# Optimization experiments

Hardware: AMD Instinct MI355X
Metric: run time of the kernel (lower is better)

The kernel has to match this reference:

```python
import jax, jax.numpy as jnp
import numpy as np

B, P, ENC = 64, 196, 512
E, H, A, V, L = 1024, 1024, 512, 20000, 25


def setup_inputs() -> dict:
    key = jax.random.key(0)
    ks = jax.random.split(key, 20)
    s = 0.02
    return {
        "encoder_out": jax.random.normal(ks[0], (B, P, ENC), jnp.float32),
        "captions": jax.random.randint(ks[1], (B, L), 0, V),
        "lengths": L,
        # attention MLP
        "W_enc_att": jax.random.normal(ks[2], (ENC, A), jnp.float32) * s,
        "b_enc_att": jnp.zeros((A,), jnp.float32),
        "W_dec_att": jax.random.normal(ks[3], (H, A), jnp.float32) * s,
        "b_dec_att": jnp.zeros((A,), jnp.float32),
        "W_full_att": jax.random.normal(ks[4], (A, 1), jnp.float32) * s,
        "b_full_att": jnp.zeros((1,), jnp.float32),
        # embedding
        "emb_table": jax.random.normal(ks[5], (V, E), jnp.float32) * s,
        # LSTMCell: input = embedding + context -> (E+ENC, 4H)
        "W_ih": jax.random.normal(ks[6], (E + ENC, 4 * H), jnp.float32) * s,
        "b_ih": jnp.zeros((4 * H,), jnp.float32),
        "W_hh": jax.random.normal(ks[7], (H, 4 * H), jnp.float32) * s,
        "b_hh": jnp.zeros((4 * H,), jnp.float32),
        # init states
        "W_init_h": jax.random.normal(ks[8], (ENC, H), jnp.float32) * s,
        "b_init_h": jnp.zeros((H,), jnp.float32),
        "W_init_c": jax.random.normal(ks[9], (ENC, H), jnp.float32) * s,
        "b_init_c": jnp.zeros((H,), jnp.float32),
        # gate + output proj
        "W_fbeta": jax.random.normal(ks[10], (H, ENC), jnp.float32) * s,
        "b_fbeta": jnp.zeros((ENC,), jnp.float32),
        "W_fc": jax.random.normal(ks[11], (H, V), jnp.float32) * s,
        "b_fc": jnp.zeros((V,), jnp.float32),
    }


def _decode(encoder_out, W_enc_att, b_enc_att, W_dec_att, b_dec_att,
            W_full_att, b_full_att, emb_table, W_ih, b_ih, W_hh, b_hh,
            W_init_h, b_init_h, W_init_c, b_init_c, W_fbeta, b_fbeta,
            W_fc, b_fc, captions, T):
    # precompute encoder-side attention projection (constant across timesteps)
    att_enc = encoder_out @ W_enc_att + b_enc_att          # (B, P, A)
    mean_feat = encoder_out.mean(axis=1)                   # (B, ENC)
    h0 = mean_feat @ W_init_h + b_init_h
    c0 = mean_feat @ W_init_c + b_init_c
    embeddings = emb_table[captions[:, :T]]                # (B, T, E)
    xs = jnp.swapaxes(embeddings, 0, 1)                    # (T, B, E)

    def step(carry, emb_t):
        h, c = carry
        att_dec = h @ W_dec_att + b_dec_att                # (B, A)
        energy = (jax.nn.relu(att_enc + att_dec[:, None, :]) @ W_full_att
                  + b_full_att)[..., 0]                    # (B, P)
        alpha = jax.nn.softmax(energy, axis=1)
        context = jnp.einsum('bp,bpe->be', alpha, encoder_out)
        gate = jax.nn.sigmoid(h @ W_fbeta + b_fbeta)       # (B, ENC)
        x = jnp.concatenate([emb_t, gate * context], axis=1)
        gates = x @ W_ih + b_ih + h @ W_hh + b_hh          # (B, 4H)
        i, f, g, o = jnp.split(gates, 4, axis=1)           # torch order i,f,g,o
        c = jax.nn.sigmoid(f) * c + jax.nn.sigmoid(i) * jnp.tanh(g)
        h = jax.nn.sigmoid(o) * jnp.tanh(c)
        preds = h @ W_fc + b_fc                            # dropout = identity (eval)
        return (h, c), (preds, alpha)

    _, (preds, alphas) = jax.lax.scan(step, (h0, c0), xs)
    predictions = jnp.swapaxes(preds, 0, 1)                # (B, T, V)
    alphas = jnp.swapaxes(alphas, 0, 1)                    # (B, T, P)
    return predictions, alphas


def reference(encoder_out, captions, lengths, W_enc_att, b_enc_att, W_dec_att,
              b_dec_att, W_full_att, b_full_att, emb_table, W_ih, b_ih, W_hh,
              b_hh, W_init_h, b_init_h, W_init_c, b_init_c, W_fbeta, b_fbeta,
              W_fc, b_fc):
    T = int(lengths) - 1
    return _decode(encoder_out, W_enc_att, b_enc_att, W_dec_att, b_dec_att,
                   W_full_att, b_full_att, emb_table, W_ih, b_ih, W_hh, b_hh,
                   W_init_h, b_init_h, W_init_c, b_init_c, W_fbeta, b_fbeta,
                   W_fc, b_fc, captions, T)
```

## Files before the change

### kernel.cpp

```cpp
#include <hip/hip_runtime.h>
#include <hip/hip_bf16.h>

#define BB 64
#define PP 196
#define ENCD 512
#define ED 1024
#define HD 1024
#define AD 512
#define VD 20000
#define TT 24
#define VPAD 20096
#define HOFF 32768

typedef __attribute__((ext_vector_type(8))) short short8;
typedef __attribute__((ext_vector_type(4))) short short4v;
typedef __attribute__((ext_vector_type(4))) float f32x4;

__device__ __forceinline__ float sigf(float x) { return 1.f / (1.f + __expf(-x)); }

__device__ __forceinline__ unsigned short f2bf(float f) {
    unsigned u = __builtin_bit_cast(unsigned, f);
    u = (u + 0x7FFFu + ((u >> 16) & 1u)) >> 16;
    return (unsigned short)u;
}
__device__ __forceinline__ void split2(float v, unsigned short& h, unsigned short& l) {
    h = f2bf(v);
    float hf = __builtin_bit_cast(float, ((unsigned)h) << 16);
    l = f2bf(v - hf);
}

__global__ __launch_bounds__(256) void split_w_kernel(
    const float* __restrict__ W, unsigned short* __restrict__ oh,
    unsigned short* __restrict__ ol, int N , int Npad, int coff,
    int Nlaunch, int rowoff, int perm) {
    int n = blockIdx.x * 256 + threadIdx.x;
    if (n >= Nlaunch) return;
    int kc = blockIdx.y;
    int src = perm ? ((n & 3) * 1024 + (n >> 2)) : n;
    short8 vh, vl;
    #pragma unroll
    for (int j = 0; j < 8; ++j) {
        float v = (src < N) ? W[(size_t)(rowoff + kc * 8 + j) * N + src] : 0.f;
        unsigned short h, l; split2(v, h, l);
        vh[j] = (short)h; vl[j] = (short)l;
    }
    size_t o = ((size_t)kc * Npad + coff + n) * 8;
    *(short8*)(oh + o) = vh; *(short8*)(ol + o) = vl;
}

__global__ __launch_bounds__(256) void embed_f32_kernel(
    const int* __restrict__ captions, const float* __restrict__ table,
    float* __restrict__ emb_f) {
    int t = blockIdx.x, b = blockIdx.y;
    int tok = captions[b * 25 + t];
    const float4* src = (const float4*)(table + (size_t)tok * ED);
    float4* dst = (float4*)(emb_f + ((size_t)t * BB + b) * ED);
    dst[threadIdx.x] = src[threadIdx.x];
}

__global__ __launch_bounds__(256) void bias_perm_kernel(
    const float* __restrict__ b_ih, const float* __restrict__ b_hh,
    float* __restrict__ out) {
    int n = blockIdx.x * 256 + threadIdx.x;
    int src = (n & 3) * 1024 + (n >> 2);
    out[n] = b_ih[src] + b_hh[src];
}

__global__ __launch_bounds__(512) void mean_kernel(const float* __restrict__ enc,
                                                   float* __restrict__ mf) {
    int b = blockIdx.x; int e = threadIdx.x;
    const float* base = enc + (size_t)b * PP * ENCD + e;
    float s = 0.f;
    #pragma unroll 4
    for (int p = 0; p < PP; ++p) s += base[(size_t)p * ENCD];
    mf[b * ENCD + e] = s * (1.f / PP);
}

__global__ __launch_bounds__(256) void init_hc_kernel(
    const float* __restrict__ mf,
    const float* __restrict__ Wh, const float* __restrict__ bh,
    const float* __restrict__ Wc, const float* __restrict__ bc,
    unsigned short* __restrict__ hc_h, unsigned short* __restrict__ hc_l,
    float* __restrict__ c0) {
    int b = blockIdx.x;
    int isC = blockIdx.y;
    const float* W    = isC ? Wc : Wh;
    const float* bias = isC ? bc : bh;
    __shared__ float smf[ENCD];
    for (int i = threadIdx.x; i < ENCD; i += 256) smf[i] = mf[b * ENCD + i];
    __syncthreads();
    #pragma unroll
    for (int jj = 0; jj < 4; ++jj) {
        int j = threadIdx.x + jj * 256;
        float acc = bias[j];
        for (int k = 0; k < ENCD; ++k) acc += smf[k] * W[(size_t)k * HD + j];
        if (isC) c0[b * HD + j] = acc;
        else {
            unsigned short h, l; split2(acc, h, l);
            size_t o = ((size_t)(j >> 3) * 64 + b) * 8 + (j & 7);
            hc_h[o] = h; hc_l[o] = l;
        }
    }
}

__global__ __launch_bounds__(256) void mfma_gemm_bigf(
    const float* __restrict__ Ap,
    const unsigned short* __restrict__ Bh, const unsigned short* __restrict__ Bl,
    const float* __restrict__ bias, float* __restrict__ C,
    int N, int Npad, int K, int Mtiles, int Ntiles, int inner_m) {
    __shared__ __align__(16) short lds[32768];
    short* Ahs = lds;
    short* Als = lds + 8192;
    short* Bhs = lds + 16384;
    short* Bls = lds + 24576;
    int tid = threadIdx.x, lane = tid & 63, w = tid >> 6;
    int nwg = Mtiles * Ntiles;
    int orig = blockIdx.x;
    int q = nwg >> 3, r = nwg & 7;
    int xcd = orig & 7;
    int basew = (xcd < r) ? xcd * (q + 1) : r * (q + 1) + (xcd - r) * q;
    int wg = basew + (orig >> 3);
    int mt, nt;
    if (inner_m) { mt = wg % Mtiles; nt = wg / Mtiles; }
    else         { nt = wg % Ntiles; mt = wg / Ntiles; }
    int m0 = mt * 128, n0 = nt * 128;
    int wr = w >> 1, wc = w & 1;
    f32x4 acc[4][4];
    #pragma unroll
    for (int i = 0; i < 4; ++i)
        #pragma unroll
        for (int j = 0; j < 4; ++j) acc[i][j] = (f32x4){0.f, 0.f, 0.f, 0.f};
    int nsteps = K >> 6;
    float4 va[8];
    short8 rb[2][4];
    auto load_step = [&](int s) {
        int k0 = s * 64, kc0 = s * 8;
        #pragma unroll
        for (int it = 0; it < 8; ++it) {
            int idx = it * 256 + tid; int m = idx >> 4, k4 = idx & 15;
            va[it] = *(const float4*)(Ap + (size_t)(m0 + m) * K + k0 + k4 * 4);
        }
        #pragma unroll
        for (int it = 0; it < 4; ++it) {
            int g = w * 4 + it; int kcl = g >> 1; int rb0 = (g & 1) * 64;
            size_t gb = ((size_t)(kc0 + kcl) * Npad + n0 + rb0 + lane) * 8;
            rb[0][it] = *(const short8*)(Bh + gb);
            rb[1][it] = *(const short8*)(Bl + gb);
        }
    };
    load_step(0);
    for (int s = 0; s < nsteps; ++s) {
        __syncthreads();
        #pragma unroll
        for (int it = 0; it < 8; ++it) {
            int idx = it * 256 + tid; int m = idx >> 4, k4 = idx & 15;
            int kc = k4 >> 1, jh = (k4 & 1) * 4;
            float vv[4] = {va[it].x, va[it].y, va[it].z, va[it].w};
            short4v hv, lv;
            #pragma unroll
            for (int qq = 0; qq < 4; ++qq) {
                unsigned short h, l; split2(vv[qq], h, l);
                hv[qq] = (short)h; lv[qq] = (short)l;
            }
            int o = kc * 1024 + ((m ^ kc) << 3) + jh;
            *(short4v*)(Ahs + o) = hv;
            *(short4v*)(Als + o) = lv;
        }
        #pragma unroll
        for (int it = 0; it < 4; ++it) {
            int g = w * 4 + it; int kcl = g >> 1; int rb0 = (g & 1) * 64;
            int o = (kcl * 128 + rb0 + lane) * 8;
            *(short8*)(Bhs + o) = rb[0][it];
            *(short8*)(Bls + o) = rb[1][it];
        }
        __syncthreads();
        if (s + 1 < nsteps) load_step(s + 1);
        #pragma unroll
        for (int ks = 0; ks < 2; ++ks) {
            int kq = ks * 4 + (lane >> 4);
            short8 afh[4], afl[4], bfh[4], bfl[4];
            #pragma unroll
            for (int mi = 0; mi < 4; ++mi) {
                int row = wr * 64 + mi * 16 + (lane & 15);
                int o = kq * 1024 + ((row ^ kq) << 3);
                afh[mi] = *(const short8*)(Ahs + o);
                afl[mi] = *(const short8*)(Als + o);
            }
            #pragma unroll
            for (int ni = 0; ni < 4; ++ni) {
                int o = (kq * 128 + wc * 64 + ni * 16 + (lane & 15)) * 8;
                bfh[ni] = *(const short8*)(Bhs + o);
                bfl[ni] = *(const short8*)(Bls + o);
            }
            #pragma unroll
            for (int mi = 0; mi < 4; ++mi)
                #pragma unroll
                for (int ni = 0; ni < 4; ++ni) {
                    acc[mi][ni] = __builtin_amdgcn_mfma_f32_16x16x32_bf16(afh[mi], bfh[ni], acc[mi][ni], 0, 0, 0);
                    acc[mi][ni] = __builtin_amdgcn_mfma_f32_16x16x32_bf16(afh[mi], bfl[ni], acc[mi][ni], 0, 0, 0);
                    acc[mi][ni] = __builtin_amdgcn_mfma_f32_16x16x32_bf16(afl[mi], bfh[ni], acc[mi][ni], 0, 0, 0);
                }
        }
    }
    #pragma unroll
    for (int mi = 0; mi < 4; ++mi) {
        int rrow = m0 + wr * 64 + mi * 16 + ((lane >> 4) << 2);
        #pragma unroll
        for (int ni = 0; ni < 4; ++ni) {
            int c = n0 + wc * 64 + ni * 16 + (lane & 15);
            if (c < N) {
                float bv = bias ? bias[c] : 0.f;
                #pragma unroll
                for (int qq = 0; qq < 4; ++qq)
                    C[(size_t)(rrow + qq) * N + c] = acc[mi][ni][qq] + bv;
            }
        }
    }
}

__global__ __launch_bounds__(256) void mfma_gemm_small(
    const unsigned short* __restrict__ A0h, const unsigned short* __restrict__ A0l,
    const unsigned short* __restrict__ B0h, const unsigned short* __restrict__ B0l,
    float* __restrict__ out, int Npad, int steps) {
    __shared__ __align__(16) short lds[24576];
    short* Ahs = lds;
    short* Als = lds + 4096;
    short* Bhs = lds + 8192;
    short* Bls = lds + 16384;
    int tid = threadIdx.x, lane = tid & 63, w = tid >> 6;
    int n0 = blockIdx.x * 128;
    int kc_base = blockIdx.y * steps * 8;
    out += (size_t)blockIdx.y * 64 * Npad;
    f32x4 acc[4][2];
    #pragma unroll
    for (int i = 0; i < 4; ++i)
        #pragma unroll
        for (int j = 0; j < 2; ++j) acc[i][j] = (f32x4){0.f, 0.f, 0.f, 0.f};
    short8 raa[2][2], rbb[2][4];
    auto load_step = [&](int s) {
        int kc0 = kc_base + s * 8;
        #pragma unroll
        for (int it = 0; it < 2; ++it) {
            int kcl = w * 2 + it; size_t off = ((size_t)(kc0 + kcl) * 64 + lane) * 8;
            raa[0][it] = *(const short8*)(A0h + off);
            raa[1][it] = *(const short8*)(A0l + off);
        }
        #pragma unroll
        for (int it = 0; it < 4; ++it) {
            int g = w * 4 + it; int kcl = g >> 1; int cb = (g & 1) * 64;
            size_t off = ((size_t)(kc0 + kcl) * Npad + n0 + cb + lane) * 8;
            rbb[0][it] = *(const short8*)(B0h + off);
            rbb[1][it] = *(const short8*)(B0l + off);
        }
    };
    load_step(0);
    for (int s = 0; s < steps; ++s) {
        __syncthreads();
        #pragma unroll
        for (int it = 0; it < 2; ++it) {
            int kcl = w * 2 + it; int o = (kcl * 64 + lane) * 8;
            *(short8*)(Ahs + o) = raa[0][it];
            *(short8*)(Als + o) = raa[1][it];
        }
        #pragma unroll
        for (int it = 0; it < 4; ++it) {
            int g = w * 4 + it; int kcl = g >> 1; int cb = (g & 1) * 64;
            int o = (kcl * 128 + cb + lane) * 8;
            *(short8*)(Bhs + o) = rbb[0][it];
            *(short8*)(Bls + o) = rbb[1][it];
        }
        __syncthreads();
        if (s + 1 < steps) load_step(s + 1);
        #pragma unroll
        for (int ks = 0; ks < 2; ++ks) {
            int kq = ks * 4 + (lane >> 4);
            short8 afh[4], afl[4], bfh[2], bfl[2];
            #pragma unroll
            for (int mi = 0; mi < 4; ++mi) {
                int o = (kq * 64 + mi * 16 + (lane & 15)) * 8;
                afh[mi] = *(const short8*)(Ahs + o);
                afl[mi] = *(const short8*)(Als + o);
            }
            #pragma unroll
            for (int ni = 0; ni < 2; ++ni) {
                int o = (kq * 128 + w * 32 + ni * 16 + (lane & 15)) * 8;
                bfh[ni] = *(const short8*)(Bhs + o);
                bfl[ni] = *(const short8*)(Bls + o);
            }
            #pragma unroll
            for (int mi = 0; mi < 4; ++mi)
                #pragma unroll
                for (int ni = 0; ni < 2; ++ni) {
                    acc[mi][ni] = __builtin_amdgcn_mfma_f32_16x16x32_bf16(afh[mi], bfh[ni], acc[mi][ni], 0, 0, 0);
                    acc[mi][ni] = __builtin_amdgcn_mfma_f32_16x16x32_bf16(afh[mi], bfl[ni], acc[mi][ni], 0, 0, 0);
                    acc[mi][ni] = __builtin_amdgcn_mfma_f32_16x16x32_bf16(afl[mi], bfh[ni], acc[mi][ni], 0, 0, 0);
                }
        }
    }
    #pragma unroll
    for (int mi = 0; mi < 4; ++mi) {
        int rrow = mi * 16 + ((lane >> 4) << 2);
        #pragma unroll
        for (int ni = 0; ni < 2; ++ni) {
            int c = n0 + w * 32 + ni * 16 + (lane & 15);
            #pragma unroll
            for (int qq = 0; qq < 4; ++qq)
                out[(size_t)(rrow + qq) * Npad + c] = acc[mi][ni][qq];
        }
    }
}

__global__ __launch_bounds__(1024) void attn_ctx_kernel(
    const float* __restrict__ att_enc, const float* __restrict__ adg,
    const float* __restrict__ b_dec, const float* __restrict__ Wfull,
    const float* __restrict__ enc, const float* __restrict__ b_fbeta,
    float* __restrict__ alpha_out, unsigned short* __restrict__ x2h,
    unsigned short* __restrict__ x2l, int t) {
    int b = blockIdx.x; int tid = threadIdx.x;
    __shared__ float sdec[AD], sw[AD], sgate[AD], sal[256], sE[256], red[256];
    __shared__ float sctx[2][AD];
    if (tid < AD) {
        float s = b_dec[tid];
        #pragma unroll
        for (int ks = 0; ks < 8; ++ks) s += adg[((size_t)ks * BB + b) * 1024 + tid];
        sdec[tid] = s;
        sw[tid] = Wfull[tid];
    } else {
        int e = tid - AD;
        float s = b_fbeta[e];
        #pragma unroll
        for (int ks = 0; ks < 8; ++ks) s += adg[((size_t)ks * BB + b) * 1024 + AD + e];
        sgate[e] = s;
    }
    __syncthreads();
    int w = tid >> 6, lane = tid & 63;
    float4 sd0 = *(const float4*)&sdec[lane * 8];
    float4 sd1 = *(const float4*)&sdec[lane * 8 + 4];
    float4 sw0 = *(const float4*)&sw[lane * 8];
    float4 sw1 = *(const float4*)&sw[lane * 8 + 4];
    for (int p = w; p < PP; p += 16) {
        const float* row = att_enc + ((size_t)b * PP + p) * AD + lane * 8;
        float4 v0 = *(const float4*)row;
        float4 v1 = *(const float4*)(row + 4);
        float part = fmaxf(v0.x + sd0.x, 0.f) * sw0.x + fmaxf(v0.y + sd0.y, 0.f) * sw0.y +
                     fmaxf(v0.z + sd0.z, 0.f) * sw0.z + fmaxf(v0.w + sd0.w, 0.f) * sw0.w +
                     fmaxf(v1.x + sd1.x, 0.f) * sw1.x + fmaxf(v1.y + sd1.y, 0.f) * sw1.y +
                     fmaxf(v1.z + sd1.z, 0.f) * sw1.z + fmaxf(v1.w + sd1.w, 0.f) * sw1.w;
        #pragma unroll
        for (int off = 32; off > 0; off >>= 1) part += __shfl_down(part, off, 64);
        if (lane == 0) sE[p] = part;
    }
    __syncthreads();
    float myE = (tid < PP) ? sE[tid] : -1e30f;
    if (tid < 256) red[tid] = myE;
    __syncthreads();
    for (int s = 128; s > 0; s >>= 1) {
        if (tid < s) red[tid] = fmaxf(red[tid], red[tid + s]);
        __syncthreads();
    }
    float mx = red[0];
    __syncthreads();
    float ex = (tid < PP) ? __expf(myE - mx) : 0.f;
    if (tid < 256) red[tid] = ex;
    __syncthreads();
    for (int s = 128; s > 0; s >>= 1) {
        if (tid < s) red[tid] += red[tid + s];
        __syncthreads();
    }
    if (tid < PP) {
        float al = ex * (1.f / red[0]);
        sal[tid] = al;
        alpha_out[((size_t)b * TT + t) * PP + tid] = al;
    }
    __syncthreads();
    int e = tid & 511, half = tid >> 9;
    const float* basep = enc + (size_t)b * PP * ENCD + e;
    float s2 = 0.f;
    #pragma unroll 2
    for (int p = half * 98; p < half * 98 + 98; ++p) s2 += sal[p] * basep[(size_t)p * ENCD];
    sctx[half][e] = s2;
    __syncthreads();
    if (tid < AD) {
        float ctx = sctx[0][tid] + sctx[1][tid];
        float gate = sigf(sgate[tid]);
        unsigned short h, l; split2(gate * ctx, h, l);
        size_t o = ((size_t)(tid >> 3) * 64 + b) * 8 + (tid & 7);
        x2h[o] = h; x2l[o] = l;
    }
}

__global__ __launch_bounds__(128) void gates_lstm_kernel(
    const unsigned short* __restrict__ Ah, const unsigned short* __restrict__ Al,
    const unsigned short* __restrict__ Bh, const unsigned short* __restrict__ Bl,
    const float* __restrict__ pregates, float* __restrict__ c,
    unsigned short* __restrict__ ho_h, unsigned short* __restrict__ ho_l,
    float* __restrict__ h_all, int t) {
    __shared__ __align__(16) short lds[10240];
    __shared__ float gl[64][17];
    short* Ahs = lds;
    short* Als = lds + 4096;
    short* Bhs = lds + 8192;
    short* Bls = lds + 9216;
    int tid = threadIdx.x, lane = tid & 63, w = tid >> 6;
    int n0 = blockIdx.x * 16;
    f32x4 acc[4];
    #pragma unroll
    for (int i = 0; i < 4; ++i) acc[i] = (f32x4){0.f, 0.f, 0.f, 0.f};
    short8 ra[2][4], rb[2];
    auto load_step = [&](int s) {
        int kc0 = s * 8;
        #pragma unroll
        for (int it = 0; it < 4; ++it) {
            int idx = it * 128 + tid; int kcl = idx >> 6, row = idx & 63;
            size_t off = ((size_t)(kc0 + kcl) * 64 + row) * 8;
            ra[0][it] = *(const short8*)(Ah + off);
            ra[1][it] = *(const short8*)(Al + off);
        }
        {
            int kcl = tid >> 4, col = tid & 15;
            size_t off = ((size_t)(kc0 + kcl) * 4096 + n0 + col) * 8;
            rb[0] = *(const short8*)(Bh + off);
            rb[1] = *(const short8*)(Bl + off);
        }
    };
    load_step(0);
    for (int s = 0; s < 24; ++s) {
        __syncthreads();
        #pragma unroll
        for (int it = 0; it < 4; ++it) {
            int idx = it * 128 + tid; int kcl = idx >> 6, row = idx & 63;
            int o = (kcl * 64 + row) * 8;
            *(short8*)(Ahs + o) = ra[0][it];
            *(short8*)(Als + o) = ra[1][it];
        }
        {
            int kcl = tid >> 4, col = tid & 15;
            int o = (kcl * 16 + col) * 8;
            *(short8*)(Bhs + o) = rb[0];
            *(short8*)(Bls + o) = rb[1];
        }
        __syncthreads();
        if (s + 1 < 24) load_step(s + 1);
        int kq = w * 4 + (lane >> 4);
        short8 afh[4], afl[4], bfh, bfl;
        #pragma unroll
        for (int mi = 0; mi < 4; ++mi) {
            int o = (kq * 64 + mi * 16 + (lane & 15)) * 8;
            afh[mi] = *(const short8*)(Ahs + o);
            afl[mi] = *(const short8*)(Als + o);
        }
        int ob = (kq * 16 + (lane & 15)) * 8;
        bfh = *(const short8*)(Bhs + ob);
        bfl = *(const short8*)(Bls + ob);
        #pragma unroll
        for (int mi = 0; mi < 4; ++mi) {
            acc[mi] = __builtin_amdgcn_mfma_f32_16x16x32_bf16(afh[mi], bfh, acc[mi], 0, 0, 0);
            acc[mi] = __builtin_amdgcn_mfma_f32_16x16x32_bf16(afh[mi], bfl, acc[mi], 0, 0, 0);
            acc[mi] = __builtin_amdgcn_mfma_f32_16x16x32_bf16(afl[mi], bfh, acc[mi], 0, 0, 0);
        }
    }
    if (w == 0) {
        #pragma unroll
        for (int mi = 0; mi < 4; ++mi)
            #pragma unroll
            for (int qq = 0; qq < 4; ++qq)
                gl[mi * 16 + ((lane >> 4) << 2) + qq][lane & 15] = acc[mi][qq];
    }
    __syncthreads();
    if (w == 1) {
        #pragma unroll
        for (int mi = 0; mi < 4; ++mi)
            #pragma unroll
            for (int qq = 0; qq < 4; ++qq) {
                int r = mi * 16 + ((lane >> 4) << 2) + qq, cl = lane & 15;
                gl[r][cl] += acc[mi][qq] + pregates[((size_t)(t * 64 + r)) * 4096 + n0 + cl];
            }
    }
    __syncthreads();
    #pragma unroll
    for (int i = 0; i < 2; ++i) {
        int idx = tid + i * 128;
        int bb = idx >> 2, jl = idx & 3;
        float iG = gl[bb][4 * jl + 0], fG = gl[bb][4 * jl + 1];
        float gG = gl[bb][4 * jl + 2], oG = gl[bb][4 * jl + 3];
        int j = (n0 >> 2) + jl;
        float cn = sigf(fG) * c[bb * HD + j] + sigf(iG) * tanhf(gG);
        c[bb * HD + j] = cn;
        float hn = sigf(oG) * tanhf(cn);
        unsigned short h, l; split2(hn, h, l);
        size_t o1 = ((size_t)(j >> 3) * 64 + bb) * 8 + (j & 7);
        ho_h[o1] = h; ho_l[o1] = l;
        h_all[((size_t)bb * TT + t) * HD + j] = hn;
    }
}

extern "C" void kernel_launch(void* const* d_in, const int* in_sizes, int n_in,
                              void* d_out, int out_size, void* d_ws, size_t ws_size,
                              hipStream_t stream) {
    const float* enc      = (const float*)d_in[0];
    const int*   captions = (const int*)d_in[1];
    const float* W_enc    = (const float*)d_in[3];
    const float* b_enc    = (const float*)d_in[4];
    const float* W_dec    = (const float*)d_in[5];
    const float* b_dec    = (const float*)d_in[6];
    const float* W_full   = (const float*)d_in[7];
    const float* table    = (const float*)d_in[9];
    const float* W_ih     = (const float*)d_in[10];
    const float* b_ih     = (const float*)d_in[11];
    const float* W_hh     = (const float*)d_in[12];
    const float* b_hh     = (const float*)d_in[13];
    const float* W_init_h = (const float*)d_in[14];
    const float* b_init_h = (const float*)d_in[15];
    const float* W_init_c = (const float*)d_in[16];
    const float* b_init_c = (const float*)d_in[17];
    const float* W_fbeta  = (const float*)d_in[18];
    const float* b_fbeta  = (const float*)d_in[19];
    const float* W_fc     = (const float*)d_in[20];
    const float* b_fc     = (const float*)d_in[21];

    float* preds  = (float*)d_out;
    float* alphas = (float*)d_out + (size_t)BB * TT * VD;

    char* base = (char*)d_ws;
    size_t off = 0;
    auto take = [&](size_t b) { void* r = (void*)(base + off); off += (b + 255) & ~(size_t)255; return r; };
    float* att_enc = (float*)take((size_t)12544 * 512 * 4);
    unsigned short* wih1_h = (unsigned short*)take((size_t)128 * 4096 * 8 * 2);
    unsigned short* wih1_l = (unsigned short*)take((size_t)128 * 4096 * 8 * 2);
    unsigned short* wg2_h  = (unsigned short*)take((size_t)192 * 4096 * 8 * 2);
    unsigned short* wg2_l  = (unsigned short*)take((size_t)192 * 4096 * 8 * 2);
    unsigned short* watt_h = (unsigned short*)take((size_t)128 * 1024 * 8 * 2);
    unsigned short* watt_l = (unsigned short*)take((size_t)128 * 1024 * 8 * 2);
    unsigned short* wenc_h = (unsigned short*)take((size_t)64 * 512 * 8 * 2);
    unsigned short* wenc_l = (unsigned short*)take((size_t)64 * 512 * 8 * 2);
    float* pregates = (float*)take((size_t)TT * BB * 4096 * 4);
    float* adg      = (float*)take((size_t)8 * BB * 1024 * 4);
    float* emb_f    = (float*)take((size_t)TT * BB * ED * 4);
    float* biasp    = (float*)take((size_t)4096 * 4);
    unsigned short* wfc_h = (unsigned short*)(base);
    unsigned short* wfc_l = (unsigned short*)(base + (size_t)128 * VPAD * 8 * 2);
    float* c_buf = (float*)take((size_t)BB * HD * 4);
    float* mf    = (float*)take((size_t)BB * ENCD * 4);
    unsigned short* axh_h[2], *axh_l[2];
    axh_h[0] = (unsigned short*)take((size_t)192 * 64 * 8 * 2);
    axh_l[0] = (unsigned short*)take((size_t)192 * 64 * 8 * 2);
    axh_h[1] = (unsigned short*)take((size_t)192 * 64 * 8 * 2);
    axh_l[1] = (unsigned short*)take((size_t)192 * 64 * 8 * 2);
    float* h_all = (float*)take((size_t)TT * BB * HD * 4);

    split_w_kernel<<<dim3(2, 64), 256, 0, stream>>>(W_enc, wenc_h, wenc_l, 512, 512, 0, 512, 0, 0);
    split_w_kernel<<<dim3(2, 128), 256, 0, stream>>>(W_dec, watt_h, watt_l, 512, 1024, 0, 512, 0, 0);
    split_w_kernel<<<dim3(2, 128), 256, 0, stream>>>(W_fbeta, watt_h, watt_l, 512, 1024, 512, 512, 0, 0);
    split_w_kernel<<<dim3(16, 128), 256, 0, stream>>>(W_ih, wih1_h, wih1_l, 4096, 4096, 0, 4096, 0, 1);
    split_w_kernel<<<dim3(16, 64), 256, 0, stream>>>(W_ih, wg2_h, wg2_l, 4096, 4096, 0, 4096, 1024, 1);
    split_w_kernel<<<dim3(16, 128), 256, 0, stream>>>(W_hh, wg2_h + (size_t)64 * 4096 * 8,
                                                      wg2_l + (size_t)64 * 4096 * 8,
                                                      4096, 4096, 0, 4096, 0, 1);
    bias_perm_kernel<<<16, 256, 0, stream>>>(b_ih, b_hh, biasp);
    embed_f32_kernel<<<dim3(TT, BB), 256, 0, stream>>>(captions, table, emb_f);
    mean_kernel<<<BB, 512, 0, stream>>>(enc, mf);
    init_hc_kernel<<<dim3(BB, 2), 256, 0, stream>>>(mf, W_init_h, b_init_h, W_init_c, b_init_c,
                                                    axh_h[0] + HOFF, axh_l[0] + HOFF, c_buf);
    mfma_gemm_bigf<<<392, 256, 0, stream>>>(enc, wenc_h, wenc_l, b_enc, att_enc,
                                            512, 512, 512, 98, 4, 0);
    mfma_gemm_bigf<<<384, 256, 0, stream>>>(emb_f, wih1_h, wih1_l, biasp, pregates,
                                            4096, 4096, 1024, 12, 32, 1);

    for (int t = 0; t < TT; ++t) {
        int par = t & 1;
        mfma_gemm_small<<<dim3(8, 8), 256, 0, stream>>>(
            axh_h[par] + HOFF, axh_l[par] + HOFF, watt_h, watt_l, adg, 1024, 2);
        attn_ctx_kernel<<<BB, 1024, 0, stream>>>(att_enc, adg, b_dec, W_full, enc, b_fbeta,
                                                 alphas, axh_h[par], axh_l[par], t);
        gates_lstm_kernel<<<256, 128, 0, stream>>>(
            axh_h[par], axh_l[par], wg2_h, wg2_l, pregates, c_buf,
            axh_h[1 - par] + HOFF, axh_l[1 - par] + HOFF, h_all, t);
    }

    split_w_kernel<<<dim3(79, 128), 256, 0, stream>>>(W_fc, wfc_h, wfc_l, VD, VPAD, 0, VPAD, 0, 0);
    mfma_gemm_bigf<<<1884, 256, 0, stream>>>(h_all, wfc_h, wfc_l, b_fc, preds,
                                             VD, VPAD, 1024, 12, 157, 1);
}
```

Measured before the change: 1.622 ms.

## Hoist h@W_hh into the attention GEMM and shrink the recurrent gate GEMM

The h·W_hh product is moved out of the per-step gate GEMM and concatenated with W_dec and W_fbeta into one wide weight (N=5120), computed in a single split-K GEMM with more blocks. The gate kernel now multiplies only the context part (K=512) of W_ih, then adds the precomputed W_hh partials from adg along with pregates. Both per-step GEMMs drop the LDS staging and load MFMA fragments straight from global memory. The aim is to spread the serial per-step work across more CUs and cut the critical-path length. In exchange, the gate kernel reads 8 split-K partial sums per element, and emb_f is aliased onto adg, which relies on the embeddings being consumed before the loop overwrites that buffer.

Result: faster. 1.532 ms (-5.6%).

```diff
diff --git a/kernel.cpp b/kernel.cpp
--- a/kernel.cpp
+++ b/kernel.cpp
@@ -218,94 +218,53 @@
     }
 }
 
-__global__ __launch_bounds__(256) void mfma_gemm_small(
-    const unsigned short* __restrict__ A0h, const unsigned short* __restrict__ A0l,
-    const unsigned short* __restrict__ B0h, const unsigned short* __restrict__ B0l,
-    float* __restrict__ out, int Npad, int steps) {
-    __shared__ __align__(16) short lds[24576];
-    short* Ahs = lds;
-    short* Als = lds + 4096;
-    short* Bhs = lds + 8192;
-    short* Bls = lds + 16384;
+__global__ __launch_bounds__(256) void hgemm_direct(
+    const unsigned short* __restrict__ Ah, const unsigned short* __restrict__ Al,
+    const unsigned short* __restrict__ Bh, const unsigned short* __restrict__ Bl,
+    float* __restrict__ out ) {
     int tid = threadIdx.x, lane = tid & 63, w = tid >> 6;
-    int n0 = blockIdx.x * 128;
-    int kc_base = blockIdx.y * steps * 8;
-    out += (size_t)blockIdx.y * 64 * Npad;
+    int n0 = blockIdx.x * 128 + w * 32;
+    int kc0 = blockIdx.y * 16;
+    out += (size_t)blockIdx.y * 64 * 5120;
     f32x4 acc[4][2];
     #pragma unroll
     for (int i = 0; i < 4; ++i)
         #pragma unroll
         for (int j = 0; j < 2; ++j) acc[i][j] = (f32x4){0.f, 0.f, 0.f, 0.f};
-    short8 raa[2][2], rbb[2][4];
-    auto load_step = [&](int s) {
-        int kc0 = kc_base + s * 8;
-        #pragma unroll
-        for (int it = 0; it < 2; ++it) {
-            int kcl = w * 2 + it; size_t off = ((size_t)(kc0 + kcl) * 64 + lane) * 8;
-            raa[0][it] = *(const short8*)(A0h + off);
-            raa[1][it] = *(const short8*)(A0l + off);
-        }
-        #pragma unroll
-        for (int it = 0; it < 4; ++it) {
-            int g = w * 4 + it; int kcl = g >> 1; int cb = (g & 1) * 64;
-            size_t off = ((size_t)(kc0 + kcl) * Npad + n0 + cb + lane) * 8;
-            rbb[0][it] = *(const short8*)(B0h + off);
-            rbb[1][it] = *(const short8*)(B0l + off);
-        }
-    };
-    load_step(0);
-    for (int s = 0; s < steps; ++s) {
-        __syncthreads();
-        #pragma unroll
-        for (int it = 0; it < 2; ++it) {
-            int kcl = w * 2 + it; int o = (kcl * 64 + lane) * 8;
-            *(short8*)(Ahs + o) = raa[0][it];
-            *(short8*)(Als + o) = raa[1][it];
-        }
-        #pragma unroll
-        for (int it = 0; it < 4; ++it) {
-            int g = w * 4 + it; int kcl = g >> 1; int cb = (g & 1) * 64;
-            int o = (kcl * 128 + cb + lane) * 8;
-            *(short8*)(Bhs + o) = rbb[0][it];
-            *(short8*)(Bls + o) = rbb[1][it];
-        }
-        __syncthreads();
-        if (s + 1 < steps) load_step(s + 1);
-        #pragma unroll
-        for (int ks = 0; ks < 2; ++ks) {
-            int kq = ks * 4 + (lane >> 4);
-            short8 afh[4], afl[4], bfh[2], bfl[2];
-            #pragma unroll
-            for (int mi = 0; mi < 4; ++mi) {
-                int o = (kq * 64 + mi * 16 + (lane & 15)) * 8;
-                afh[mi] = *(const short8*)(Ahs + o);
-                afl[mi] = *(const short8*)(Als + o);
+    #pragma unroll
+    for (int s = 0; s < 4; ++s) {
+        int kc = kc0 + s * 4 + (lane >> 4);
+        short8 afh[4], afl[4], bfh[2], bfl[2];
+        #pragma unroll
+        for (int mi = 0; mi < 4; ++mi) {
+            size_t o = ((size_t)kc * 64 + mi * 16 + (lane & 15)) * 8;
+            afh[mi] = *(const short8*)(Ah + o);
+            afl[mi] = *(const short8*)(Al + o);
+        }
+        #pragma unroll
+        for (int ni = 0; ni < 2; ++ni) {
+            size_t o = ((size_t)kc * 5120 + n0 + ni * 16 + (lane & 15)) * 8;
+            bfh[ni] = *(const short8*)(Bh + o);
+            bfl[ni] = *(const short8*)(Bl + o);
+        }
+        #pragma unroll
+        for (int mi = 0; mi < 4; ++mi)
+            #pragma unroll
+            for (int ni = 0; ni < 2; ++ni) {
+                acc[mi][ni] = __builtin_amdgcn_mfma_f32_16x16x32_bf16(afh[mi], bfh[ni], acc[mi][ni], 0, 0, 0);
+                acc[mi][ni] = __builtin_amdgcn_mfma_f32_16x16x32_bf16(afh[mi], bfl[ni], acc[mi][ni], 0, 0, 0);
+                acc[mi][ni] = __builtin_amdgcn_mfma_f32_16x16x32_bf16(afl[mi], bfh[ni], acc[mi][ni], 0, 0, 0);
             }
-            #pragma unroll
-            for (int ni = 0; ni < 2; ++ni) {
-                int o = (kq * 128 + w * 32 + ni * 16 + (lane & 15)) * 8;
-                bfh[ni] = *(const short8*)(Bhs + o);
-                bfl[ni] = *(const short8*)(Bls + o);
-            }
-            #pragma unroll
-            for (int mi = 0; mi < 4; ++mi)
-                #pragma unroll
-                for (int ni = 0; ni < 2; ++ni) {
-                    acc[mi][ni] = __builtin_amdgcn_mfma_f32_16x16x32_bf16(afh[mi], bfh[ni], acc[mi][ni], 0, 0, 0);
-                    acc[mi][ni] = __builtin_amdgcn_mfma_f32_16x16x32_bf16(afh[mi], bfl[ni], acc[mi][ni], 0, 0, 0);
-                    acc[mi][ni] = __builtin_amdgcn_mfma_f32_16x16x32_bf16(afl[mi], bfh[ni], acc[mi][ni], 0, 0, 0);
-                }
-        }
     }
     #pragma unroll
     for (int mi = 0; mi < 4; ++mi) {
         int rrow = mi * 16 + ((lane >> 4) << 2);
         #pragma unroll
         for (int ni = 0; ni < 2; ++ni) {
-            int c = n0 + w * 32 + ni * 16 + (lane & 15);
+            int c = n0 + ni * 16 + (lane & 15);
             #pragma unroll
             for (int qq = 0; qq < 4; ++qq)
-                out[(size_t)(rrow + qq) * Npad + c] = acc[mi][ni][qq];
+                out[(size_t)(rrow + qq) * 5120 + c] = acc[mi][ni][qq];
         }
     }
 }
@@ -322,14 +281,14 @@
     if (tid < AD) {
         float s = b_dec[tid];
         #pragma unroll
-        for (int ks = 0; ks < 8; ++ks) s += adg[((size_t)ks * BB + b) * 1024 + tid];
+        for (int ks = 0; ks < 8; ++ks) s += adg[((size_t)ks * BB + b) * 5120 + tid];
         sdec[tid] = s;
         sw[tid] = Wfull[tid];
     } else {
         int e = tid - AD;
         float s = b_fbeta[e];
         #pragma unroll
-        for (int ks = 0; ks < 8; ++ks) s += adg[((size_t)ks * BB + b) * 1024 + AD + e];
+        for (int ks = 0; ks < 8; ++ks) s += adg[((size_t)ks * BB + b) * 5120 + 512 + e];
         sgate[e] = s;
     }
     __syncthreads();
@@ -389,108 +348,83 @@
     }
 }
 
-__global__ __launch_bounds__(128) void gates_lstm_kernel(
+__global__ __launch_bounds__(256) void gates_lstm2(
     const unsigned short* __restrict__ Ah, const unsigned short* __restrict__ Al,
     const unsigned short* __restrict__ Bh, const unsigned short* __restrict__ Bl,
-    const float* __restrict__ pregates, float* __restrict__ c,
-    unsigned short* __restrict__ ho_h, unsigned short* __restrict__ ho_l,
-    float* __restrict__ h_all, int t) {
-    __shared__ __align__(16) short lds[10240];
-    __shared__ float gl[64][17];
-    short* Ahs = lds;
-    short* Als = lds + 4096;
-    short* Bhs = lds + 8192;
-    short* Bls = lds + 9216;
+    const float* __restrict__ pregates, const float* __restrict__ adg,
+    float* __restrict__ c, unsigned short* __restrict__ ho_h,
+    unsigned short* __restrict__ ho_l, float* __restrict__ h_all, int t) {
+    __shared__ float gl[4][64][33];
     int tid = threadIdx.x, lane = tid & 63, w = tid >> 6;
-    int n0 = blockIdx.x * 16;
-    f32x4 acc[4];
-    #pragma unroll
-    for (int i = 0; i < 4; ++i) acc[i] = (f32x4){0.f, 0.f, 0.f, 0.f};
-    short8 ra[2][4], rb[2];
-    auto load_step = [&](int s) {
-        int kc0 = s * 8;
-        #pragma unroll
-        for (int it = 0; it < 4; ++it) {
-            int idx = it * 128 + tid; int kcl = idx >> 6, row = idx & 63;
-            size_t off = ((size_t)(kc0 + kcl) * 64 + row) * 8;
-            ra[0][it] = *(const short8*)(Ah + off);
-            ra[1][it] = *(const short8*)(Al + off);
-        }
+    int n0 = blockIdx.x * 32;
+    f32x4 acc[4][2];
+    #pragma unroll
+    for (int i = 0; i < 4; ++i)
+        #pragma unroll
+        for (int j = 0; j < 2; ++j) acc[i][j] = (f32x4){0.f, 0.f, 0.f, 0.f};
+    #pragma unroll
+    for (int s = 0; s < 4; ++s) {
+        int kc = w * 16 + s * 4 + (lane >> 4);
+        short8 afh[4], afl[4], bfh[2], bfl[2];
+        #pragma unroll
+        for (int mi = 0; mi < 4; ++mi) {
+            size_t o = ((size_t)kc * 64 + mi * 16 + (lane & 15)) * 8;
+            afh[mi] = *(const short8*)(Ah + o);
+            afl[mi] = *(const short8*)(Al + o);
+        }
+        #pragma unroll
+        for (int ni = 0; ni < 2; ++ni) {
+            size_t o = ((size_t)kc * 4096 + n0 + ni * 16 + (lane & 15)) * 8;
+            bfh[ni] = *(const short8*)(Bh + o);
+            bfl[ni] = *(const short8*)(Bl + o);
+        }
+        #pragma unroll
+        for (int mi = 0; mi < 4; ++mi)
+            #pragma unroll
+            for (int ni = 0; ni < 2; ++ni) {
+                acc[mi][ni] = __builtin_amdgcn_mfma_f32_16x16x32_bf16(afh[mi], bfh[ni], acc[mi][ni], 0, 0, 0);
+                acc[mi][ni] = __builtin_amdgcn_mfma_f32_16x16x32_bf16(afh[mi], bfl[ni], acc[mi][ni], 0, 0, 0);
+                acc[mi][ni] = __builtin_amdgcn_mfma_f32_16x16x32_bf16(afl[mi], bfh[ni], acc[mi][ni], 0, 0, 0);
+            }
+    }
+    #pragma unroll
+    for (int mi = 0; mi < 4; ++mi) {
+        int rrow = mi * 16 + ((lane >> 4) << 2);
+        #pragma unroll
+        for (int ni = 0; ni < 2; ++ni) {
+            int cl = ni * 16 + (lane & 15);
+            #pragma unroll
+            for (int qq = 0; qq < 4; ++qq)
+                gl[w][rrow + qq][cl] = acc[mi][ni][qq];
+        }
+    }
+    __syncthreads();
+    #pragma unroll
+    for (int i = 0; i < 2; ++i) {
+        int idx = tid + i * 256;
+        int b = idx >> 3, jl = idx & 7;
+        float g4[4];
+        #pragma unroll
+        for (int qq = 0; qq < 4; ++qq)
+            g4[qq] = gl[0][b][4 * jl + qq] + gl[1][b][4 * jl + qq] +
+                     gl[2][b][4 * jl + qq] + gl[3][b][4 * jl + qq];
         {
-            int kcl = tid >> 4, col = tid & 15;
-            size_t off = ((size_t)(kc0 + kcl) * 4096 + n0 + col) * 8;
-            rb[0] = *(const short8*)(Bh + off);
-            rb[1] = *(const short8*)(Bl + off);
-        }
-    };
-    load_step(0);
-    for (int s = 0; s < 24; ++s) {
-        __syncthreads();
-        #pragma unroll
-        for (int it = 0; it < 4; ++it) {
-            int idx = it * 128 + tid; int kcl = idx >> 6, row = idx & 63;
-            int o = (kcl * 64 + row) * 8;
-            *(short8*)(Ahs + o) = ra[0][it];
-            *(short8*)(Als + o) = ra[1][it];
-        }
-        {
-            int kcl = tid >> 4, col = tid & 15;
-            int o = (kcl * 16 + col) * 8;
-            *(short8*)(Bhs + o) = rb[0];
-            *(short8*)(Bls + o) = rb[1];
-        }
-        __syncthreads();
-        if (s + 1 < 24) load_step(s + 1);
-        int kq = w * 4 + (lane >> 4);
-        short8 afh[4], afl[4], bfh, bfl;
-        #pragma unroll
-        for (int mi = 0; mi < 4; ++mi) {
-            int o = (kq * 64 + mi * 16 + (lane & 15)) * 8;
-            afh[mi] = *(const short8*)(Ahs + o);
-            afl[mi] = *(const short8*)(Als + o);
-        }
-        int ob = (kq * 16 + (lane & 15)) * 8;
-        bfh = *(const short8*)(Bhs + ob);
-        bfl = *(const short8*)(Bls + ob);
-        #pragma unroll
-        for (int mi = 0; mi < 4; ++mi) {
-            acc[mi] = __builtin_amdgcn_mfma_f32_16x16x32_bf16(afh[mi], bfh, acc[mi], 0, 0, 0);
-            acc[mi] = __builtin_amdgcn_mfma_f32_16x16x32_bf16(afh[mi], bfl, acc[mi], 0, 0, 0);
-            acc[mi] = __builtin_amdgcn_mfma_f32_16x16x32_bf16(afl[mi], bfh, acc[mi], 0, 0, 0);
-        }
-    }
-    if (w == 0) {
-        #pragma unroll
-        for (int mi = 0; mi < 4; ++mi)
-            #pragma unroll
-            for (int qq = 0; qq < 4; ++qq)
-                gl[mi * 16 + ((lane >> 4) << 2) + qq][lane & 15] = acc[mi][qq];
-    }
-    __syncthreads();
-    if (w == 1) {
-        #pragma unroll
-        for (int mi = 0; mi < 4; ++mi)
-            #pragma unroll
-            for (int qq = 0; qq < 4; ++qq) {
-                int r = mi * 16 + ((lane >> 4) << 2) + qq, cl = lane & 15;
-                gl[r][cl] += acc[mi][qq] + pregates[((size_t)(t * 64 + r)) * 4096 + n0 + cl];
-            }
-    }
-    __syncthreads();
-    #pragma unroll
-    for (int i = 0; i < 2; ++i) {
-        int idx = tid + i * 128;
-        int bb = idx >> 2, jl = idx & 3;
-        float iG = gl[bb][4 * jl + 0], fG = gl[bb][4 * jl + 1];
-        float gG = gl[bb][4 * jl + 2], oG = gl[bb][4 * jl + 3];
+            float4 pv = *(const float4*)&pregates[((size_t)(t * 64 + b)) * 4096 + n0 + 4 * jl];
+            g4[0] += pv.x; g4[1] += pv.y; g4[2] += pv.z; g4[3] += pv.w;
+        }
+        #pragma unroll
+        for (int ks = 0; ks < 8; ++ks) {
+            float4 av = *(const float4*)&adg[((size_t)ks * BB + b) * 5120 + 1024 + n0 + 4 * jl];
+            g4[0] += av.x; g4[1] += av.y; g4[2] += av.z; g4[3] += av.w;
+        }
         int j = (n0 >> 2) + jl;
-        float cn = sigf(fG) * c[bb * HD + j] + sigf(iG) * tanhf(gG);
-        c[bb * HD + j] = cn;
-        float hn = sigf(oG) * tanhf(cn);
+        float cn = sigf(g4[1]) * c[b * HD + j] + sigf(g4[0]) * tanhf(g4[2]);
+        c[b * HD + j] = cn;
+        float hn = sigf(g4[3]) * tanhf(cn);
         unsigned short h, l; split2(hn, h, l);
-        size_t o1 = ((size_t)(j >> 3) * 64 + bb) * 8 + (j & 7);
+        size_t o1 = ((size_t)(j >> 3) * 64 + b) * 8 + (j & 7);
         ho_h[o1] = h; ho_l[o1] = l;
-        h_all[((size_t)bb * TT + t) * HD + j] = hn;
+        h_all[((size_t)b * TT + t) * HD + j] = hn;
     }
 }
 
@@ -525,17 +459,17 @@
     size_t off = 0;
     auto take = [&](size_t b) { void* r = (void*)(base + off); off += (b + 255) & ~(size_t)255; return r; };
     float* att_enc = (float*)take((size_t)12544 * 512 * 4);
+    unsigned short* wbig_h = (unsigned short*)take((size_t)128 * 5120 * 8 * 2);
+    unsigned short* wbig_l = (unsigned short*)take((size_t)128 * 5120 * 8 * 2);
     unsigned short* wih1_h = (unsigned short*)take((size_t)128 * 4096 * 8 * 2);
     unsigned short* wih1_l = (unsigned short*)take((size_t)128 * 4096 * 8 * 2);
-    unsigned short* wg2_h  = (unsigned short*)take((size_t)192 * 4096 * 8 * 2);
-    unsigned short* wg2_l  = (unsigned short*)take((size_t)192 * 4096 * 8 * 2);
-    unsigned short* watt_h = (unsigned short*)take((size_t)128 * 1024 * 8 * 2);
-    unsigned short* watt_l = (unsigned short*)take((size_t)128 * 1024 * 8 * 2);
+    unsigned short* wih2_h = (unsigned short*)take((size_t)64 * 4096 * 8 * 2);
+    unsigned short* wih2_l = (unsigned short*)take((size_t)64 * 4096 * 8 * 2);
     unsigned short* wenc_h = (unsigned short*)take((size_t)64 * 512 * 8 * 2);
     unsigned short* wenc_l = (unsigned short*)take((size_t)64 * 512 * 8 * 2);
     float* pregates = (float*)take((size_t)TT * BB * 4096 * 4);
-    float* adg      = (float*)take((size_t)8 * BB * 1024 * 4);
-    float* emb_f    = (float*)take((size_t)TT * BB * ED * 4);
+    float* adg      = (float*)take((size_t)8 * BB * 5120 * 4);
+    float* emb_f    = adg;
     float* biasp    = (float*)take((size_t)4096 * 4);
     unsigned short* wfc_h = (unsigned short*)(base);
     unsigned short* wfc_l = (unsigned short*)(base + (size_t)128 * VPAD * 8 * 2);
@@ -549,13 +483,11 @@
     float* h_all = (float*)take((size_t)TT * BB * HD * 4);
 
     split_w_kernel<<<dim3(2, 64), 256, 0, stream>>>(W_enc, wenc_h, wenc_l, 512, 512, 0, 512, 0, 0);
-    split_w_kernel<<<dim3(2, 128), 256, 0, stream>>>(W_dec, watt_h, watt_l, 512, 1024, 0, 512, 0, 0);
-    split_w_kernel<<<dim3(2, 128), 256, 0, stream>>>(W_fbeta, watt_h, watt_l, 512, 1024, 512, 512, 0, 0);
+    split_w_kernel<<<dim3(2, 128), 256, 0, stream>>>(W_dec, wbig_h, wbig_l, 512, 5120, 0, 512, 0, 0);
+    split_w_kernel<<<dim3(2, 128), 256, 0, stream>>>(W_fbeta, wbig_h, wbig_l, 512, 5120, 512, 512, 0, 0);
+    split_w_kernel<<<dim3(16, 128), 256, 0, stream>>>(W_hh, wbig_h, wbig_l, 4096, 5120, 1024, 4096, 0, 1);
     split_w_kernel<<<dim3(16, 128), 256, 0, stream>>>(W_ih, wih1_h, wih1_l, 4096, 4096, 0, 4096, 0, 1);
-    split_w_kernel<<<dim3(16, 64), 256, 0, stream>>>(W_ih, wg2_h, wg2_l, 4096, 4096, 0, 4096, 1024, 1);
-    split_w_kernel<<<dim3(16, 128), 256, 0, stream>>>(W_hh, wg2_h + (size_t)64 * 4096 * 8,
-                                                      wg2_l + (size_t)64 * 4096 * 8,
-                                                      4096, 4096, 0, 4096, 0, 1);
+    split_w_kernel<<<dim3(16, 64), 256, 0, stream>>>(W_ih, wih2_h, wih2_l, 4096, 4096, 0, 4096, 1024, 1);
     bias_perm_kernel<<<16, 256, 0, stream>>>(b_ih, b_hh, biasp);
     embed_f32_kernel<<<dim3(TT, BB), 256, 0, stream>>>(captions, table, emb_f);
     mean_kernel<<<BB, 512, 0, stream>>>(enc, mf);
@@ -568,12 +500,12 @@
 
     for (int t = 0; t < TT; ++t) {
         int par = t & 1;
-        mfma_gemm_small<<<dim3(8, 8), 256, 0, stream>>>(
-            axh_h[par] + HOFF, axh_l[par] + HOFF, watt_h, watt_l, adg, 1024, 2);
+        hgemm_direct<<<dim3(40, 8), 256, 0, stream>>>(
+            axh_h[par] + HOFF, axh_l[par] + HOFF, wbig_h, wbig_l, adg);
         attn_ctx_kernel<<<BB, 1024, 0, stream>>>(att_enc, adg, b_dec, W_full, enc, b_fbeta,
                                                  alphas, axh_h[par], axh_l[par], t);
-        gates_lstm_kernel<<<256, 128, 0, stream>>>(
-            axh_h[par], axh_l[par], wg2_h, wg2_l, pregates, c_buf,
+        gates_lstm2<<<128, 256, 0, stream>>>(
+            axh_h[par], axh_l[par], wih2_h, wih2_l, pregates, adg, c_buf,
             axh_h[1 - par] + HOFF, axh_l[1 - par] + HOFF, h_all, t);
     }
 
```
